# Performance work log

Measured on AMD Instinct MI355X. Metric: run time of the kernel, lower is better.

The kernel has to match this reference:

```python
import jax, jax.numpy as jnp
import numpy as np

N_NODES = 100000
N_GRAPHS = 256
HIDDEN = 64
IN_DIM = 512


def gcn_conv(x, edge_index, W, b, n_nodes):
    """PyG GCNConv: out = D^{-1/2} (A+I) D^{-1/2} (x W) + b."""
    h = x @ W  # [N, H] -- transform first (as PyG does), messages are small
    src = jnp.concatenate([edge_index[0], jnp.arange(n_nodes)])  # add self loops
    dst = jnp.concatenate([edge_index[1], jnp.arange(n_nodes)])
    ones = jnp.ones(src.shape[0], dtype=h.dtype)
    deg = jax.ops.segment_sum(ones, dst, num_segments=n_nodes)
    dinv = jnp.where(deg > 0, jax.lax.rsqrt(deg), 0.0)
    norm = dinv[src] * dinv[dst]  # [E+N]
    msg = h[src] * norm[:, None]  # gather + scale
    out = jax.ops.segment_sum(msg, dst, num_segments=n_nodes)  # scatter-add
    return out + b


def global_mean_pool(x, batch, num_graphs):
    s = jax.ops.segment_sum(x, batch, num_segments=num_graphs)
    cnt = jax.ops.segment_sum(jnp.ones(x.shape[0], dtype=x.dtype), batch,
                              num_segments=num_graphs)
    return s / jnp.maximum(cnt, 1.0)[:, None]


def setup_inputs() -> dict:
    key = jax.random.key(0)
    ks = jax.random.split(key, 9)
    x = jax.random.normal(ks[0], (N_NODES, IN_DIM), dtype=jnp.float32)
    edge_index = jax.random.randint(ks[1], (2, 1600000), 0, N_NODES, dtype=jnp.int64) \
        if jax.config.jax_enable_x64 else jax.random.randint(ks[1], (2, 1600000), 0, N_NODES).astype(jnp.int32)
    batch = jnp.sort(jax.random.randint(ks[2], (N_NODES,), 0, N_GRAPHS))
    sc1 = 1.0 / np.sqrt(IN_DIM)
    sc2 = 1.0 / np.sqrt(HIDDEN)
    W1 = jax.random.uniform(ks[3], (IN_DIM, HIDDEN), minval=-sc1, maxval=sc1, dtype=jnp.float32)
    b1 = jnp.zeros((HIDDEN,), dtype=jnp.float32)
    W2 = jax.random.uniform(ks[4], (HIDDEN, HIDDEN), minval=-sc2, maxval=sc2, dtype=jnp.float32)
    b2 = jnp.zeros((HIDDEN,), dtype=jnp.float32)
    Wfc = jax.random.uniform(ks[5], (HIDDEN, 1), minval=-sc2, maxval=sc2, dtype=jnp.float32)
    bfc = jnp.zeros((1,), dtype=jnp.float32)
    return {"x": x, "edge_index": edge_index, "batch": batch,
            "W1": W1, "b1": b1, "W2": W2, "b2": b2, "Wfc": Wfc, "bfc": bfc}


def reference(x, edge_index, batch, W1, b1, W2, b2, Wfc, bfc):
    n = x.shape[0]
    h = jax.nn.relu(gcn_conv(x, edge_index, W1, b1, n))
    h = jax.nn.relu(gcn_conv(h, edge_index, W2, b2, n))
    g = global_mean_pool(h, batch, N_GRAPHS)  # [G, H]
    out = g @ Wfc + bfc  # [G, 1]
    return out.squeeze(-1)
```

## Files before the change

### kernel.cpp

```cpp
#include <hip/hip_runtime.h>

#define HIDDEN 64
#define IN_DIM 512
#define CAP 4096
#define NB_MAX 1024

typedef short v8s __attribute__((ext_vector_type(8)));
typedef float v4f __attribute__((ext_vector_type(4)));

static __device__ __forceinline__ unsigned short f2bf(float f) {
    unsigned int u = __float_as_uint(f);
    u = (u + 0x7FFF + ((u >> 16) & 1)) >> 16;
    return (unsigned short)u;
}
static __device__ __forceinline__ float bf2f(unsigned short u) {
    return __uint_as_float(((unsigned int)u) << 16);
}
static __device__ __forceinline__ float bflo(unsigned u) { return __uint_as_float(u << 16); }
static __device__ __forceinline__ float bfhi(unsigned u) { return __uint_as_float(u & 0xffff0000u); }

__global__ void k_init(int* cursor, float* gsum, int* gcnt,
                       unsigned short* bufA, unsigned short* bufB, int n_nodes) {
    int i = blockIdx.x * 256 + threadIdx.x;
    if (i < NB_MAX) cursor[i] = 0;
    if (i < 256) { gsum[i] = 0.f; gcnt[i] = 0; }
    if (i < 64) {
        bufA[(size_t)n_nodes * 64 + i] = 0;
        bufB[(size_t)n_nodes * 64 + i] = 0;
    }
}

__launch_bounds__(256)
__global__ void k_bin(const int* __restrict__ src, const int* __restrict__ dst,
                      int* cursor, unsigned* __restrict__ bucket_data, int n_edges) {
    __shared__ unsigned words[4096];
    __shared__ unsigned short binsh[4096];
    __shared__ int hist[NB_MAX];
    __shared__ int base[NB_MAX];
    const int tid = threadIdx.x;
    const int e0 = blockIdx.x * 4096;
    for (int i = tid; i < NB_MAX; i += 256) hist[i] = 0;
    __syncthreads();
    for (int i = tid; i < 4096; i += 256) {
        int e = e0 + i;
        if (e < n_edges) {
            int d = dst[e], s = src[e];
            words[i] = ((unsigned)s << 7) | (unsigned)(d & 127);
            int b = d >> 7;
            binsh[i] = (unsigned short)b;
            atomicAdd(&hist[b], 1);
        } else binsh[i] = 0xFFFFu;
    }
    __syncthreads();
    for (int b = tid; b < NB_MAX; b += 256) {
        int c = hist[b];
        base[b] = c ? atomicAdd(&cursor[b], c) : 0;
        hist[b] = 0;
    }
    __syncthreads();
    for (int i = tid; i < 4096; i += 256) {
        unsigned short b = binsh[i];
        if (b != 0xFFFFu) {
            int slot = atomicAdd(&hist[b], 1);
            int p = base[b] + slot;
            if (p < CAP) bucket_data[(size_t)b * CAP + p] = words[i];
        }
    }
}

__launch_bounds__(256)
__global__ void k_bexc(const int* __restrict__ cursor, int* __restrict__ bucket_base,
                       int* __restrict__ row_start, int n_nodes, int nbuck) {
    __shared__ int wsum[4];
    const int t = threadIdx.x, lane = t & 63, w = t >> 6;
    int v[4], s = 0;
#pragma unroll
    for (int k = 0; k < 4; ++k) {
        int i = t * 4 + k;
        int c = (i < nbuck) ? cursor[i] : 0;
        if (c > CAP) c = CAP;
        v[k] = s; s += c;
    }
    int inc = s;
#pragma unroll
    for (int off = 1; off < 64; off <<= 1) {
        int u = __shfl_up(inc, off, 64);
        if (lane >= off) inc += u;
    }
    if (lane == 63) wsum[w] = inc;
    __syncthreads();
    int cross = 0;
    for (int i = 0; i < w; ++i) cross += wsum[i];
    int b0 = cross + inc - s;
#pragma unroll
    for (int k = 0; k < 4; ++k) {
        int i = t * 4 + k;
        if (i < NB_MAX) bucket_base[i] = b0 + v[k];
    }
    if (t == 255) row_start[n_nodes] = cross + inc;
}

__launch_bounds__(256)
__global__ void k_csr(const unsigned* __restrict__ bucket_data, const int* __restrict__ cursor,
                      const int* __restrict__ bucket_base,
                      int* __restrict__ row_start, int* __restrict__ csr,
                      float* __restrict__ dinv, int n_nodes) {
    __shared__ unsigned words[CAP];
    __shared__ int cnt[128];
    __shared__ int loff[128];
    __shared__ int cur[128];
    __shared__ int w0sum;
    const int tid = threadIdx.x, bin = blockIdx.x, n0 = bin << 7;
    int c = cursor[bin]; if (c > CAP) c = CAP;
    const unsigned* bd = bucket_data + (size_t)bin * CAP;
    for (int i = tid; i < c; i += 256) words[i] = bd[i];
    if (tid < 128) { cnt[tid] = 0; cur[tid] = 0; }
    __syncthreads();
    for (int i = tid; i < c; i += 256) atomicAdd(&cnt[words[i] & 127], 1);
    __syncthreads();
    int val = 0, inc = 0;
    if (tid < 128) {
        const int lane = tid & 63;
        val = cnt[tid];
        inc = val;
#pragma unroll
        for (int off = 1; off < 64; off <<= 1) {
            int u = __shfl_up(inc, off, 64);
            if (lane >= off) inc += u;
        }
        if (tid == 63) w0sum = inc;
    }
    __syncthreads();
    if (tid < 128) {
        int excl = inc - val + ((tid >= 64) ? w0sum : 0);
        loff[tid] = excl;
        int n = n0 + tid;
        if (n < n_nodes) {
            row_start[n] = bucket_base[bin] + excl;
            dinv[n] = rsqrtf((float)(val + 1));
        }
    }
    __syncthreads();
    const int gbase = bucket_base[bin];
    for (int i = tid; i < c; i += 256) {
        unsigned wd = words[i];
        int d = wd & 127;
        int slot = atomicAdd(&cur[d], 1);
        csr[gbase + loff[d] + slot] = (int)(wd & 0xFFFFFF80u);
    }
}

__global__ void k_prep(const float* __restrict__ W1, const float* __restrict__ W2,
                       unsigned short* __restrict__ Wt, unsigned short* __restrict__ Wt2) {
    int idx = blockIdx.x * 256 + threadIdx.x;
    if (idx < HIDDEN * IN_DIM) {
        int n = idx >> 9, k = idx & 511;
        Wt[(size_t)n * 512 + k] = f2bf(W1[(size_t)k * 64 + n]);
    } else {
        int j = idx - HIDDEN * IN_DIM;
        int n = j >> 6, k = j & 63;
        Wt2[(size_t)n * 64 + k] = f2bf(W2[(size_t)k * 64 + n]);
    }
}

__launch_bounds__(256)
__global__ void k_gemm1m(const float* __restrict__ x, const unsigned short* __restrict__ Wt,
                         const float* __restrict__ dinv, unsigned short* __restrict__ s1,
                         int n_nodes) {
    __shared__ __align__(16) unsigned short lX[64 * 136];
    __shared__ __align__(16) unsigned short lW[64 * 136];
    const int tid  = threadIdx.x;
    const int lane = tid & 63;
    const int w    = tid >> 6;
    const int quad = lane >> 4;
    const int m16  = lane & 15;
    const int row0 = blockIdx.x * 64;

    v4f acc[4];
#pragma unroll
    for (int b = 0; b < 4; ++b) acc[b] = (v4f){0.f, 0.f, 0.f, 0.f};

    for (int kc = 0; kc < IN_DIM; kc += 128) {
        __syncthreads();
#pragma unroll
        for (int i = 0; i < 8; ++i) {
            int fidx = tid + i * 256;
            int r  = fidx >> 5;
            int c4 = fidx & 31;
            int gr = row0 + r;
            float4 v = make_float4(0.f, 0.f, 0.f, 0.f);
            if (gr < n_nodes) v = ((const float4*)(x + (size_t)gr * IN_DIM + kc))[c4];
            ushort4 u = make_ushort4(f2bf(v.x), f2bf(v.y), f2bf(v.z), f2bf(v.w));
            *(ushort4*)(lX + r * 136 + c4 * 4) = u;
        }
#pragma unroll
        for (int i = 0; i < 4; ++i) {
            int idx = tid + i * 256;
            int n  = idx >> 4;
            int c8 = idx & 15;
            uint4 u = *(const uint4*)(Wt + (size_t)n * 512 + kc + c8 * 8);
            *(uint4*)(lW + n * 136 + c8 * 8) = u;
        }
        __syncthreads();
#pragma unroll
        for (int kk = 0; kk < 128; kk += 32) {
            v8s a = *(const v8s*)(lX + (w * 16 + m16) * 136 + kk + quad * 8);
#pragma unroll
            for (int b = 0; b < 4; ++b) {
                v8s bb = *(const v8s*)(lW + (b * 16 + m16) * 136 + kk + quad * 8);
                acc[b] = __builtin_amdgcn_mfma_f32_16x16x32_bf16(a, bb, acc[b], 0, 0, 0);
            }
        }
    }
    __syncthreads();
    float* lC = (float*)lX;
#pragma unroll
    for (int b = 0; b < 4; ++b)
#pragma unroll
        for (int r = 0; r < 4; ++r) {
            int rowt = w * 16 + quad * 4 + r;
            lC[rowt * 65 + b * 16 + m16] = acc[b][r];
        }
    __syncthreads();
#pragma unroll
    for (int i = 0; i < 2; ++i) {
        int base = i * 2048 + tid * 8;
        int r = base >> 6;
        int c = base & 63;
        int gr = row0 + r;
        if (gr < n_nodes) {
            float d = dinv[gr];
            const float* p = lC + r * 65 + c;
            unsigned p0 = (unsigned)f2bf(p[0] * d) | ((unsigned)f2bf(p[1] * d) << 16);
            unsigned p1 = (unsigned)f2bf(p[2] * d) | ((unsigned)f2bf(p[3] * d) << 16);
            unsigned p2 = (unsigned)f2bf(p[4] * d) | ((unsigned)f2bf(p[5] * d) << 16);
            unsigned p3 = (unsigned)f2bf(p[6] * d) | ((unsigned)f2bf(p[7] * d) << 16);
            *(uint4*)(s1 + (size_t)gr * 64 + c) = make_uint4(p0, p1, p2, p3);
        }
    }
}

__launch_bounds__(256)
__global__ void k_agg1g2(const unsigned short* __restrict__ sin, const int* __restrict__ row_start,
                         const int* __restrict__ csr, const float* __restrict__ dinv,
                         const unsigned short* __restrict__ Wt2, const float* __restrict__ b1,
                         unsigned short* __restrict__ sout, int n_nodes) {
    __shared__ __align__(16) unsigned short lW[64 * 72];
    __shared__ __align__(16) unsigned short lA[32 * 72];
    __shared__ __align__(16) float lC[32 * 65];
    const int tid  = threadIdx.x;
    const int lane = tid & 63;
    const int wave = tid >> 6;
    const int g = lane >> 3;
    const int l = lane & 7;
    const int row0 = blockIdx.x * 32;
    const int n = row0 + wave * 8 + g;
    const bool valid = (n < n_nodes);
    const char* sp = (const char*)sin;
    const int SENTB = n_nodes << 7;

#pragma unroll
    for (int i = 0; i < 2; ++i) {
        int idx = tid + i * 256;
        int nn = idx >> 3;
        int c8 = idx & 7;
        uint4 u = *(const uint4*)(Wt2 + (size_t)nn * 64 + c8 * 8);
        *(uint4*)(lW + nn * 72 + c8 * 8) = u;
    }

    int rs = 0, re = 0;
    if (valid) { rs = row_start[n]; re = row_start[n + 1]; }

    uint4 us = *(const uint4*)(sp + (size_t)(valid ? (n << 7) : SENTB) + l * 16);
    float acc0 = bflo(us.x), acc1 = bfhi(us.x);
    float acc2 = bflo(us.y), acc3 = bfhi(us.y);
    float acc4 = bflo(us.z), acc5 = bfhi(us.z);
    float acc6 = bflo(us.w), acc7 = bfhi(us.w);

    for (int base = rs; base < re; base += 16) {
        int p0 = base + l;
        int p1 = base + 8 + l;
        int a0 = (p0 < re) ? csr[p0] : SENTB;
        int a1 = (p1 < re) ? csr[p1] : SENTB;
#pragma unroll
        for (int j = 0; j < 8; ++j) {
            int ab = __shfl(a0, g * 8 + j, 64);
            uint4 u = *(const uint4*)(sp + (size_t)(unsigned)ab + l * 16);
            acc0 += bflo(u.x); acc1 += bfhi(u.x);
            acc2 += bflo(u.y); acc3 += bfhi(u.y);
            acc4 += bflo(u.z); acc5 += bfhi(u.z);
            acc6 += bflo(u.w); acc7 += bfhi(u.w);
        }
#pragma unroll
        for (int j = 0; j < 8; ++j) {
            int ab = __shfl(a1, g * 8 + j, 64);
            uint4 u = *(const uint4*)(sp + (size_t)(unsigned)ab + l * 16);
            acc0 += bflo(u.x); acc1 += bfhi(u.x);
            acc2 += bflo(u.y); acc3 += bfhi(u.y);
            acc4 += bflo(u.z); acc5 += bfhi(u.z);
            acc6 += bflo(u.w); acc7 += bfhi(u.w);
        }
    }
    {
        float d = valid ? dinv[n] : 0.f;
        const float4 bA = ((const float4*)b1)[2 * l];
        const float4 bB = ((const float4*)b1)[2 * l + 1];
        float t0 = d * acc0, t1 = d * acc1, t2 = d * acc2, t3 = d * acc3;
        float t4 = d * acc4, t5 = d * acc5, t6 = d * acc6, t7 = d * acc7;
        float v0 = fmaxf(t0 + bA.x, 0.f), v1 = fmaxf(t1 + bA.y, 0.f);
        float v2 = fmaxf(t2 + bA.z, 0.f), v3 = fmaxf(t3 + bA.w, 0.f);
        float v4 = fmaxf(t4 + bB.x, 0.f), v5 = fmaxf(t5 + bB.y, 0.f);
        float v6 = fmaxf(t6 + bB.z, 0.f), v7 = fmaxf(t7 + bB.w, 0.f);
        unsigned q0 = (unsigned)f2bf(v0) | ((unsigned)f2bf(v1) << 16);
        unsigned q1 = (unsigned)f2bf(v2) | ((unsigned)f2bf(v3) << 16);
        unsigned q2 = (unsigned)f2bf(v4) | ((unsigned)f2bf(v5) << 16);
        unsigned q3 = (unsigned)f2bf(v6) | ((unsigned)f2bf(v7) << 16);
        int r = wave * 8 + g;
        *(uint4*)(lA + r * 72 + l * 8) = make_uint4(q0, q1, q2, q3);
    }
    __syncthreads();
    {
        const int m16  = lane & 15;
        const int quad = lane >> 4;
        const int mt  = wave >> 1;
        const int nt0 = (wave & 1) * 2;
        v4f c0 = (v4f){0.f, 0.f, 0.f, 0.f};
        v4f c1 = (v4f){0.f, 0.f, 0.f, 0.f};
#pragma unroll
        for (int kk = 0; kk < 64; kk += 32) {
            v8s a  = *(const v8s*)(lA + (mt * 16 + m16) * 72 + kk + quad * 8);
            v8s b0 = *(const v8s*)(lW + (nt0 * 16 + m16) * 72 + kk + quad * 8);
            v8s b1v = *(const v8s*)(lW + ((nt0 + 1) * 16 + m16) * 72 + kk + quad * 8);
            c0 = __builtin_amdgcn_mfma_f32_16x16x32_bf16(a, b0, c0, 0, 0, 0);
            c1 = __builtin_amdgcn_mfma_f32_16x16x32_bf16(a, b1v, c1, 0, 0, 0);
        }
#pragma unroll
        for (int r = 0; r < 4; ++r) {
            int rowt = mt * 16 + quad * 4 + r;
            lC[rowt * 65 + nt0 * 16 + m16]       = c0[r];
            lC[rowt * 65 + (nt0 + 1) * 16 + m16] = c1[r];
        }
    }
    __syncthreads();
    {
        int base = tid * 8;
        int r = base >> 6;
        int c = base & 63;
        int gr = row0 + r;
        if (gr < n_nodes) {
            float d = dinv[gr];
            const float* p = lC + r * 65 + c;
            unsigned p0 = (unsigned)f2bf(p[0] * d) | ((unsigned)f2bf(p[1] * d) << 16);
            unsigned p1 = (unsigned)f2bf(p[2] * d) | ((unsigned)f2bf(p[3] * d) << 16);
            unsigned p2 = (unsigned)f2bf(p[4] * d) | ((unsigned)f2bf(p[5] * d) << 16);
            unsigned p3 = (unsigned)f2bf(p[6] * d) | ((unsigned)f2bf(p[7] * d) << 16);
            *(uint4*)(sout + (size_t)gr * 64 + c) = make_uint4(p0, p1, p2, p3);
        }
    }
}

__launch_bounds__(256)
__global__ void k_layer2pool(const unsigned short* __restrict__ sin, const int* __restrict__ row_start,
                             const int* __restrict__ csr, const float* __restrict__ b2,
                             const float* __restrict__ dinv, const float* __restrict__ Wfc,
                             const int* __restrict__ batch,
                             float* gsum, int* gcnt, int n_nodes) {
    __shared__ float lsum[256];
    __shared__ int   lcnt[256];
    const int tid = threadIdx.x;
    lsum[tid] = 0.f; lcnt[tid] = 0;
    __syncthreads();
    const int lane = tid & 63;
    const int wave = tid >> 6;
    const int g = lane >> 3;
    const int l = lane & 7;
    const int n = (blockIdx.x * 4 + wave) * 8 + g;
    const bool valid = (n < n_nodes);
    const char* sp = (const char*)sin;
    const int SENTB = n_nodes << 7;

    int rs = 0, re = 0;
    if (valid) { rs = row_start[n]; re = row_start[n + 1]; }

    uint4 us = *(const uint4*)(sp + (size_t)(valid ? (n << 7) : SENTB) + l * 16);
    float acc0 = bflo(us.x), acc1 = bfhi(us.x);
    float acc2 = bflo(us.y), acc3 = bfhi(us.y);
    float acc4 = bflo(us.z), acc5 = bfhi(us.z);
    float acc6 = bflo(us.w), acc7 = bfhi(us.w);

    for (int base = rs; base < re; base += 16) {
        int p0 = base + l;
        int p1 = base + 8 + l;
        int a0 = (p0 < re) ? csr[p0] : SENTB;
        int a1 = (p1 < re) ? csr[p1] : SENTB;
#pragma unroll
        for (int j = 0; j < 8; ++j) {
            int ab = __shfl(a0, g * 8 + j, 64);
            uint4 u = *(const uint4*)(sp + (size_t)(unsigned)ab + l * 16);
            acc0 += bflo(u.x); acc1 += bfhi(u.x);
            acc2 += bflo(u.y); acc3 += bfhi(u.y);
            acc4 += bflo(u.z); acc5 += bfhi(u.z);
            acc6 += bflo(u.w); acc7 += bfhi(u.w);
        }
#pragma unroll
        for (int j = 0; j < 8; ++j) {
            int ab = __shfl(a1, g * 8 + j, 64);
            uint4 u = *(const uint4*)(sp + (size_t)(unsigned)ab + l * 16);
            acc0 += bflo(u.x); acc1 += bfhi(u.x);
            acc2 += bflo(u.y); acc3 += bfhi(u.y);
            acc4 += bflo(u.z); acc5 += bfhi(u.z);
            acc6 += bflo(u.w); acc7 += bfhi(u.w);
        }
    }
    float d = dinv[valid ? n : 0];
    const float4 bA  = ((const float4*)b2)[2 * l];
    const float4 bB  = ((const float4*)b2)[2 * l + 1];
    const float4 wA  = ((const float4*)Wfc)[2 * l];
    const float4 wB  = ((const float4*)Wfc)[2 * l + 1];
    float t = fmaxf(fmaf(d, acc0, bA.x), 0.f) * wA.x
            + fmaxf(fmaf(d, acc1, bA.y), 0.f) * wA.y
            + fmaxf(fmaf(d, acc2, bA.z), 0.f) * wA.z
            + fmaxf(fmaf(d, acc3, bA.w), 0.f) * wA.w
            + fmaxf(fmaf(d, acc4, bB.x), 0.f) * wB.x
            + fmaxf(fmaf(d, acc5, bB.y), 0.f) * wB.y
            + fmaxf(fmaf(d, acc6, bB.z), 0.f) * wB.z
            + fmaxf(fmaf(d, acc7, bB.w), 0.f) * wB.w;
#pragma unroll
    for (int off = 4; off; off >>= 1) t += __shfl_down(t, off, 8);
    if (l == 0 && valid) {
        int gr = batch[n];
        atomicAdd(&lsum[gr], t);
        atomicAdd(&lcnt[gr], 1);
    }
    __syncthreads();
    if (lcnt[tid]) {
        atomicAdd(&gsum[tid], lsum[tid]);
        atomicAdd(&gcnt[tid], lcnt[tid]);
    }
}

__global__ void k_out(const float* __restrict__ gsum, const int* __restrict__ gcnt,
                      const float* __restrict__ bfc, float* out) {
    int g = threadIdx.x;
    if (g < 256) {
        float c = (float)(gcnt[g] > 1 ? gcnt[g] : 1);
        out[g] = gsum[g] / c + bfc[0];
    }
}

extern "C" void kernel_launch(void* const* d_in, const int* in_sizes, int n_in,
                              void* d_out, int out_size, void* d_ws, size_t ws_size,
                              hipStream_t stream) {
    const float* x   = (const float*)d_in[0];
    const int*   ei  = (const int*)d_in[1];
    const int*   bat = (const int*)d_in[2];
    const float* W1  = (const float*)d_in[3];
    const float* b1  = (const float*)d_in[4];
    const float* W2  = (const float*)d_in[5];
    const float* b2  = (const float*)d_in[6];
    const float* Wfc = (const float*)d_in[7];
    const float* bfc = (const float*)d_in[8];
    float* out = (float*)d_out;

    const int n_nodes = in_sizes[2];
    const int n_edges = in_sizes[1] / 2;
    const int* src = ei;
    const int* dst = ei + n_edges;
    const int NBUCK = (n_nodes + 127) >> 7;

    char* w = (char*)d_ws;
    size_t off = 0;
    auto alloc = [&](size_t bytes) -> void* {
        void* p = w + off;
        off += (bytes + 255) & ~(size_t)255;
        return p;
    };
    float* dinv = (float*)alloc((size_t)n_nodes * sizeof(float));
    unsigned short* bufA = (unsigned short*)alloc(((size_t)n_nodes + 1) * HIDDEN * 2);
    unsigned short* bufB = (unsigned short*)alloc(((size_t)n_nodes + 1) * HIDDEN * 2);
    unsigned short* Wt   = (unsigned short*)alloc((size_t)HIDDEN * IN_DIM * 2);
    unsigned short* Wt2  = (unsigned short*)alloc((size_t)HIDDEN * HIDDEN * 2);
    float* gsum = (float*)alloc(256 * sizeof(float));
    int*   gcnt = (int*)  alloc(256 * sizeof(int));
    int*   cursor      = (int*)alloc((size_t)NB_MAX * sizeof(int));
    int*   bucket_base = (int*)alloc((size_t)NB_MAX * sizeof(int));
    unsigned* bucket_data = (unsigned*)alloc((size_t)NB_MAX * CAP * sizeof(unsigned));
    int* row_start = (int*)alloc(((size_t)n_nodes + 1) * sizeof(int));
    int* csr       = (int*)alloc(((size_t)n_edges + 64) * sizeof(int));
    (void)ws_size; (void)n_in; (void)out_size;

    hipLaunchKernelGGL(k_init, dim3(NB_MAX / 256), dim3(256), 0, stream,
                       cursor, gsum, gcnt, bufA, bufB, n_nodes);
    hipLaunchKernelGGL(k_bin, dim3((n_edges + 4095) / 4096), dim3(256), 0, stream,
                       src, dst, cursor, bucket_data, n_edges);
    hipLaunchKernelGGL(k_bexc, dim3(1), dim3(256), 0, stream,
                       cursor, bucket_base, row_start, n_nodes, NBUCK);
    hipLaunchKernelGGL(k_csr, dim3(NBUCK), dim3(256), 0, stream,
                       bucket_data, cursor, bucket_base, row_start, csr, dinv, n_nodes);
    hipLaunchKernelGGL(k_prep, dim3((HIDDEN * IN_DIM + HIDDEN * HIDDEN) / 256), dim3(256), 0, stream,
                       W1, W2, Wt, Wt2);
    hipLaunchKernelGGL(k_gemm1m, dim3((n_nodes + 63) / 64), dim3(256), 0, stream,
                       x, Wt, dinv, bufA, n_nodes);
    hipLaunchKernelGGL(k_agg1g2, dim3((n_nodes + 31) / 32), dim3(256), 0, stream,
                       bufA, row_start, csr, dinv, Wt2, b1, bufB, n_nodes);
    hipLaunchKernelGGL(k_layer2pool, dim3((n_nodes + 31) / 32), dim3(256), 0, stream,
                       bufB, row_start, csr, b2, dinv, Wfc, bat, gsum, gcnt, n_nodes);
    hipLaunchKernelGGL(k_out, dim3(1), dim3(256), 0, stream, gsum, gcnt, bfc, out);
}
```

Measured before the change: 415.3 us.

## Sort nodes by degree bucket to balance aggregation wave workloads

Builds a degree histogram during CSR construction, scans it, and produces a permutation that groups nodes with similar in-degree. Both aggregation kernels then process nodes in this permuted order, so the 8 nodes sharing a wave have similar edge counts and less lane divergence. This adds two small kernels and an extra indirection per node, and it scatters the output writes and the batch/dinv reads, which costs memory locality.

```diff
diff --git a/kernel.cpp b/kernel.cpp
--- a/kernel.cpp
+++ b/kernel.cpp
@@ -4,6 +4,7 @@
 #define IN_DIM 512
 #define CAP 4096
 #define NB_MAX 1024
+#define DBINS 512
 
 typedef short v8s __attribute__((ext_vector_type(8)));
 typedef float v4f __attribute__((ext_vector_type(4)));
@@ -20,10 +21,11 @@
 static __device__ __forceinline__ float bfhi(unsigned u) { return __uint_as_float(u & 0xffff0000u); }
 
 __global__ void k_init(int* cursor, float* gsum, int* gcnt,
-                       unsigned short* bufA, unsigned short* bufB, int n_nodes) {
+                       unsigned short* bufA, unsigned short* bufB, int* ghist, int n_nodes) {
     int i = blockIdx.x * 256 + threadIdx.x;
     if (i < NB_MAX) cursor[i] = 0;
     if (i < 256) { gsum[i] = 0.f; gcnt[i] = 0; }
+    if (i < DBINS) ghist[i] = 0;
     if (i < 64) {
         bufA[(size_t)n_nodes * 64 + i] = 0;
         bufB[(size_t)n_nodes * 64 + i] = 0;
@@ -104,17 +106,19 @@
 __global__ void k_csr(const unsigned* __restrict__ bucket_data, const int* __restrict__ cursor,
                       const int* __restrict__ bucket_base,
                       int* __restrict__ row_start, int* __restrict__ csr,
-                      float* __restrict__ dinv, int n_nodes) {
+                      float* __restrict__ dinv, int* __restrict__ ghist, int n_nodes) {
     __shared__ unsigned words[CAP];
     __shared__ int cnt[128];
     __shared__ int loff[128];
     __shared__ int cur[128];
+    __shared__ int dhist[DBINS];
     __shared__ int w0sum;
     const int tid = threadIdx.x, bin = blockIdx.x, n0 = bin << 7;
     int c = cursor[bin]; if (c > CAP) c = CAP;
     const unsigned* bd = bucket_data + (size_t)bin * CAP;
     for (int i = tid; i < c; i += 256) words[i] = bd[i];
     if (tid < 128) { cnt[tid] = 0; cur[tid] = 0; }
+    for (int i = tid; i < DBINS; i += 256) dhist[i] = 0;
     __syncthreads();
     for (int i = tid; i < c; i += 256) atomicAdd(&cnt[words[i] & 127], 1);
     __syncthreads();
@@ -138,15 +142,75 @@
         if (n < n_nodes) {
             row_start[n] = bucket_base[bin] + excl;
             dinv[n] = rsqrtf((float)(val + 1));
-        }
-    }
-    __syncthreads();
+            int cb = (val + 15) >> 4;
+            atomicAdd(&dhist[cb], 1);
+        }
+    }
+    __syncthreads();
+    for (int b = tid; b < DBINS; b += 256)
+        if (dhist[b]) atomicAdd(&ghist[b], dhist[b]);
     const int gbase = bucket_base[bin];
     for (int i = tid; i < c; i += 256) {
         unsigned wd = words[i];
         int d = wd & 127;
         int slot = atomicAdd(&cur[d], 1);
         csr[gbase + loff[d] + slot] = (int)(wd & 0xFFFFFF80u);
+    }
+}
+
+__launch_bounds__(256)
+__global__ void k_cscan(const int* __restrict__ ghist, int* __restrict__ dcur) {
+    __shared__ int wsum[4];
+    const int t = threadIdx.x, lane = t & 63, w = t >> 6;
+    int v0 = ghist[2 * t], v1 = ghist[2 * t + 1];
+    int s = v0 + v1;
+    int inc = s;
+#pragma unroll
+    for (int off = 1; off < 64; off <<= 1) {
+        int u = __shfl_up(inc, off, 64);
+        if (lane >= off) inc += u;
+    }
+    if (lane == 63) wsum[w] = inc;
+    __syncthreads();
+    int cross = 0;
+    for (int i = 0; i < w; ++i) cross += wsum[i];
+    int b0 = cross + inc - s;
+    dcur[2 * t] = b0;
+    dcur[2 * t + 1] = b0 + v0;
+}
+
+__launch_bounds__(256)
+__global__ void k_cplace(const int* __restrict__ row_start, int* dcur,
+                         int* __restrict__ perm, int n_nodes) {
+    __shared__ int lh[DBINS];
+    __shared__ int lbase[DBINS];
+    __shared__ int lcur[DBINS];
+    const int tid = threadIdx.x;
+    const int n0 = blockIdx.x * 4096;
+    for (int i = tid; i < DBINS; i += 256) lh[i] = 0;
+    __syncthreads();
+    for (int i = tid; i < 4096; i += 256) {
+        int n = n0 + i;
+        if (n < n_nodes) {
+            int deg = row_start[n + 1] - row_start[n];
+            atomicAdd(&lh[(deg + 15) >> 4], 1);
+        }
+    }
+    __syncthreads();
+    for (int b = tid; b < DBINS; b += 256) {
+        int cnt = lh[b];
+        lbase[b] = cnt ? atomicAdd(&dcur[b], cnt) : 0;
+        lcur[b] = 0;
+    }
+    __syncthreads();
+    for (int i = tid; i < 4096; i += 256) {
+        int n = n0 + i;
+        if (n < n_nodes) {
+            int deg = row_start[n + 1] - row_start[n];
+            int cb = (deg + 15) >> 4;
+            int slot = atomicAdd(&lcur[cb], 1);
+            perm[lbase[cb] + slot] = n;
+        }
     }
 }
 
@@ -244,6 +308,7 @@
 __global__ void k_agg1g2(const unsigned short* __restrict__ sin, const int* __restrict__ row_start,
                          const int* __restrict__ csr, const float* __restrict__ dinv,
                          const unsigned short* __restrict__ Wt2, const float* __restrict__ b1,
+                         const int* __restrict__ perm,
                          unsigned short* __restrict__ sout, int n_nodes) {
     __shared__ __align__(16) unsigned short lW[64 * 72];
     __shared__ __align__(16) unsigned short lA[32 * 72];
@@ -254,8 +319,9 @@
     const int g = lane >> 3;
     const int l = lane & 7;
     const int row0 = blockIdx.x * 32;
-    const int n = row0 + wave * 8 + g;
-    const bool valid = (n < n_nodes);
+    const int gid = row0 + wave * 8 + g;
+    const bool valid = (gid < n_nodes);
+    const int n = valid ? perm[gid] : 0;
     const char* sp = (const char*)sin;
     const int SENTB = n_nodes << 7;
 
@@ -346,8 +412,9 @@
         int base = tid * 8;
         int r = base >> 6;
         int c = base & 63;
-        int gr = row0 + r;
-        if (gr < n_nodes) {
+        int gid2 = row0 + r;
+        if (gid2 < n_nodes) {
+            int gr = perm[gid2];
             float d = dinv[gr];
             const float* p = lC + r * 65 + c;
             unsigned p0 = (unsigned)f2bf(p[0] * d) | ((unsigned)f2bf(p[1] * d) << 16);
@@ -363,7 +430,7 @@
 __global__ void k_layer2pool(const unsigned short* __restrict__ sin, const int* __restrict__ row_start,
                              const int* __restrict__ csr, const float* __restrict__ b2,
                              const float* __restrict__ dinv, const float* __restrict__ Wfc,
-                             const int* __restrict__ batch,
+                             const int* __restrict__ batch, const int* __restrict__ perm,
                              float* gsum, int* gcnt, int n_nodes) {
     __shared__ float lsum[256];
     __shared__ int   lcnt[256];
@@ -374,8 +441,9 @@
     const int wave = tid >> 6;
     const int g = lane >> 3;
     const int l = lane & 7;
-    const int n = (blockIdx.x * 4 + wave) * 8 + g;
-    const bool valid = (n < n_nodes);
+    const int gid = (blockIdx.x * 4 + wave) * 8 + g;
+    const bool valid = (gid < n_nodes);
+    const int n = valid ? perm[gid] : 0;
     const char* sp = (const char*)sin;
     const int SENTB = n_nodes << 7;
 
@@ -412,7 +480,7 @@
             acc6 += bflo(u.w); acc7 += bfhi(u.w);
         }
     }
-    float d = dinv[valid ? n : 0];
+    float d = dinv[n];
     const float4 bA  = ((const float4*)b2)[2 * l];
     const float4 bB  = ((const float4*)b2)[2 * l + 1];
     const float4 wA  = ((const float4*)Wfc)[2 * l];
@@ -484,26 +552,32 @@
     int*   gcnt = (int*)  alloc(256 * sizeof(int));
     int*   cursor      = (int*)alloc((size_t)NB_MAX * sizeof(int));
     int*   bucket_base = (int*)alloc((size_t)NB_MAX * sizeof(int));
+    int*   ghist       = (int*)alloc((size_t)DBINS * sizeof(int));
+    int*   dcur        = (int*)alloc((size_t)DBINS * sizeof(int));
+    int*   perm        = (int*)alloc((size_t)n_nodes * sizeof(int));
     unsigned* bucket_data = (unsigned*)alloc((size_t)NB_MAX * CAP * sizeof(unsigned));
     int* row_start = (int*)alloc(((size_t)n_nodes + 1) * sizeof(int));
     int* csr       = (int*)alloc(((size_t)n_edges + 64) * sizeof(int));
     (void)ws_size; (void)n_in; (void)out_size;
 
     hipLaunchKernelGGL(k_init, dim3(NB_MAX / 256), dim3(256), 0, stream,
-                       cursor, gsum, gcnt, bufA, bufB, n_nodes);
+                       cursor, gsum, gcnt, bufA, bufB, ghist, n_nodes);
     hipLaunchKernelGGL(k_bin, dim3((n_edges + 4095) / 4096), dim3(256), 0, stream,
                        src, dst, cursor, bucket_data, n_edges);
     hipLaunchKernelGGL(k_bexc, dim3(1), dim3(256), 0, stream,
                        cursor, bucket_base, row_start, n_nodes, NBUCK);
     hipLaunchKernelGGL(k_csr, dim3(NBUCK), dim3(256), 0, stream,
-                       bucket_data, cursor, bucket_base, row_start, csr, dinv, n_nodes);
+                       bucket_data, cursor, bucket_base, row_start, csr, dinv, ghist, n_nodes);
+    hipLaunchKernelGGL(k_cscan, dim3(1), dim3(256), 0, stream, ghist, dcur);
+    hipLaunchKernelGGL(k_cplace, dim3((n_nodes + 4095) / 4096), dim3(256), 0, stream,
+                       row_start, dcur, perm, n_nodes);
     hipLaunchKernelGGL(k_prep, dim3((HIDDEN * IN_DIM + HIDDEN * HIDDEN) / 256), dim3(256), 0, stream,
                        W1, W2, Wt, Wt2);
     hipLaunchKernelGGL(k_gemm1m, dim3((n_nodes + 63) / 64), dim3(256), 0, stream,
                        x, Wt, dinv, bufA, n_nodes);
     hipLaunchKernelGGL(k_agg1g2, dim3((n_nodes + 31) / 32), dim3(256), 0, stream,
-                       bufA, row_start, csr, dinv, Wt2, b1, bufB, n_nodes);
+                       bufA, row_start, csr, dinv, Wt2, b1, perm, bufB, n_nodes);
     hipLaunchKernelGGL(k_layer2pool, dim3((n_nodes + 31) / 32), dim3(256), 0, stream,
-                       bufB, row_start, csr, b2, dinv, Wfc, bat, gsum, gcnt, n_nodes);
+                       bufB, row_start, csr, b2, dinv, Wfc, bat, perm, gsum, gcnt, n_nodes);
     hipLaunchKernelGGL(k_out, dim3(1), dim3(256), 0, stream, gsum, gcnt, bfc, out);
 }
```

Measured after the change: 434.5 us. 1.05x slower.

## Partition CSR neighbor lists into four source-range slices for gather locality

Applied to the files above, without the earlier changes.

The CSR build now sub-sorts each node's neighbors into four slices by source node index and records four segment starts per node in a new rs4 array. Both aggregation kernels walk these segments in order, so waves running at the same time tend to gather from the same quarter of the feature table, which may improve L2 hit rates. The gather loop also changes from 16 edges per iteration to 8, with the next index block prefetched. The cost is four tail-padded segments per node instead of one, which means more masked sentinel loads for low-degree nodes, plus extra atomics and shared memory in the CSR build.

```diff
diff --git a/kernel.cpp b/kernel.cpp
--- a/kernel.cpp
+++ b/kernel.cpp
@@ -70,7 +70,8 @@
 
 __launch_bounds__(256)
 __global__ void k_bexc(const int* __restrict__ cursor, int* __restrict__ bucket_base,
-                       int* __restrict__ row_start, int n_nodes, int nbuck) {
+                       int* __restrict__ row_start, int* __restrict__ rs4,
+                       int n_nodes, int nbuck) {
     __shared__ int wsum[4];
     const int t = threadIdx.x, lane = t & 63, w = t >> 6;
     int v[4], s = 0;
@@ -97,31 +98,42 @@
         int i = t * 4 + k;
         if (i < NB_MAX) bucket_base[i] = b0 + v[k];
     }
-    if (t == 255) row_start[n_nodes] = cross + inc;
+    if (t == 255) {
+        row_start[n_nodes] = cross + inc;
+        rs4[4 * n_nodes]   = cross + inc;
+    }
 }
 
 __launch_bounds__(256)
 __global__ void k_csr(const unsigned* __restrict__ bucket_data, const int* __restrict__ cursor,
                       const int* __restrict__ bucket_base,
-                      int* __restrict__ row_start, int* __restrict__ csr,
-                      float* __restrict__ dinv, int n_nodes) {
+                      int* __restrict__ row_start, int* __restrict__ rs4, int* __restrict__ csr,
+                      float* __restrict__ dinv, int n_nodes, float inv_slice) {
     __shared__ unsigned words[CAP];
-    __shared__ int cnt[128];
-    __shared__ int loff[128];
-    __shared__ int cur[128];
+    __shared__ int cnt4[512];
+    __shared__ int loff4[512];
+    __shared__ int cur4[512];
     __shared__ int w0sum;
     const int tid = threadIdx.x, bin = blockIdx.x, n0 = bin << 7;
     int c = cursor[bin]; if (c > CAP) c = CAP;
     const unsigned* bd = bucket_data + (size_t)bin * CAP;
     for (int i = tid; i < c; i += 256) words[i] = bd[i];
-    if (tid < 128) { cnt[tid] = 0; cur[tid] = 0; }
-    __syncthreads();
-    for (int i = tid; i < c; i += 256) atomicAdd(&cnt[words[i] & 127], 1);
-    __syncthreads();
-    int val = 0, inc = 0;
+    for (int i = tid; i < 512; i += 256) { cnt4[i] = 0; cur4[i] = 0; }
+    __syncthreads();
+    for (int i = tid; i < c; i += 256) {
+        unsigned wd = words[i];
+        int d = wd & 127;
+        int q = (int)((float)(wd >> 7) * inv_slice);
+        q = q > 3 ? 3 : q;
+        atomicAdd(&cnt4[d * 4 + q], 1);
+    }
+    __syncthreads();
+    int v0 = 0, v1 = 0, v2 = 0, v3 = 0, val = 0, inc = 0;
     if (tid < 128) {
         const int lane = tid & 63;
-        val = cnt[tid];
+        v0 = cnt4[tid * 4]; v1 = cnt4[tid * 4 + 1];
+        v2 = cnt4[tid * 4 + 2]; v3 = cnt4[tid * 4 + 3];
+        val = v0 + v1 + v2 + v3;
         inc = val;
 #pragma unroll
         for (int off = 1; off < 64; off <<= 1) {
@@ -133,10 +145,17 @@
     __syncthreads();
     if (tid < 128) {
         int excl = inc - val + ((tid >= 64) ? w0sum : 0);
-        loff[tid] = excl;
+        int B = bucket_base[bin];
+        loff4[tid * 4]     = excl;
+        loff4[tid * 4 + 1] = excl + v0;
+        loff4[tid * 4 + 2] = excl + v0 + v1;
+        loff4[tid * 4 + 3] = excl + v0 + v1 + v2;
         int n = n0 + tid;
         if (n < n_nodes) {
-            row_start[n] = bucket_base[bin] + excl;
+            row_start[n] = B + excl;
+            int4 r4 = make_int4(B + excl, B + excl + v0,
+                                B + excl + v0 + v1, B + excl + v0 + v1 + v2);
+            *(int4*)(rs4 + 4 * n) = r4;
             dinv[n] = rsqrtf((float)(val + 1));
         }
     }
@@ -145,8 +164,10 @@
     for (int i = tid; i < c; i += 256) {
         unsigned wd = words[i];
         int d = wd & 127;
-        int slot = atomicAdd(&cur[d], 1);
-        csr[gbase + loff[d] + slot] = (int)(wd & 0xFFFFFF80u);
+        int q = (int)((float)(wd >> 7) * inv_slice);
+        q = q > 3 ? 3 : q;
+        int slot = atomicAdd(&cur4[d * 4 + q], 1);
+        csr[gbase + loff4[d * 4 + q] + slot] = (int)(wd & 0xFFFFFF80u);
     }
 }
 
@@ -241,7 +262,7 @@
 }
 
 __launch_bounds__(256)
-__global__ void k_agg1g2(const unsigned short* __restrict__ sin, const int* __restrict__ row_start,
+__global__ void k_agg1g2(const unsigned short* __restrict__ sin, const int* __restrict__ rs4,
                          const int* __restrict__ csr, const float* __restrict__ dinv,
                          const unsigned short* __restrict__ Wt2, const float* __restrict__ b1,
                          unsigned short* __restrict__ sout, int n_nodes) {
@@ -268,8 +289,12 @@
         *(uint4*)(lW + nn * 72 + c8 * 8) = u;
     }
 
-    int rs = 0, re = 0;
-    if (valid) { rs = row_start[n]; re = row_start[n + 1]; }
+    int4 r4 = make_int4(0, 0, 0, 0);
+    int rend = 0;
+    if (valid) {
+        r4 = *(const int4*)(rs4 + 4 * n);
+        rend = rs4[4 * n + 4];
+    }
 
     uint4 us = *(const uint4*)(sp + (size_t)(valid ? (n << 7) : SENTB) + l * 16);
     float acc0 = bflo(us.x), acc1 = bfhi(us.x);
@@ -277,30 +302,28 @@
     float acc4 = bflo(us.z), acc5 = bfhi(us.z);
     float acc6 = bflo(us.w), acc7 = bfhi(us.w);
 
-    for (int base = rs; base < re; base += 16) {
-        int p0 = base + l;
-        int p1 = base + 8 + l;
-        int a0 = (p0 < re) ? csr[p0] : SENTB;
-        int a1 = (p1 < re) ? csr[p1] : SENTB;
-#pragma unroll
-        for (int j = 0; j < 8; ++j) {
-            int ab = __shfl(a0, g * 8 + j, 64);
-            uint4 u = *(const uint4*)(sp + (size_t)(unsigned)ab + l * 16);
-            acc0 += bflo(u.x); acc1 += bfhi(u.x);
-            acc2 += bflo(u.y); acc3 += bfhi(u.y);
-            acc4 += bflo(u.z); acc5 += bfhi(u.z);
-            acc6 += bflo(u.w); acc7 += bfhi(u.w);
-        }
-#pragma unroll
-        for (int j = 0; j < 8; ++j) {
-            int ab = __shfl(a1, g * 8 + j, 64);
-            uint4 u = *(const uint4*)(sp + (size_t)(unsigned)ab + l * 16);
-            acc0 += bflo(u.x); acc1 += bfhi(u.x);
-            acc2 += bflo(u.y); acc3 += bfhi(u.y);
-            acc4 += bflo(u.z); acc5 += bfhi(u.z);
-            acc6 += bflo(u.w); acc7 += bfhi(u.w);
-        }
-    }
+    auto gather_seg = [&](int rs, int re) {
+        int a0 = (rs + l < re) ? csr[rs + l] : SENTB;
+        for (int base = rs; base < re; base += 8) {
+            int nb = base + 8;
+            int na0 = (nb + l < re) ? csr[nb + l] : SENTB;
+#pragma unroll
+            for (int j = 0; j < 8; ++j) {
+                int ab = __shfl(a0, g * 8 + j, 64);
+                uint4 u = *(const uint4*)(sp + (size_t)(unsigned)ab + l * 16);
+                acc0 += bflo(u.x); acc1 += bfhi(u.x);
+                acc2 += bflo(u.y); acc3 += bfhi(u.y);
+                acc4 += bflo(u.z); acc5 += bfhi(u.z);
+                acc6 += bflo(u.w); acc7 += bfhi(u.w);
+            }
+            a0 = na0;
+        }
+    };
+    gather_seg(r4.x, r4.y);
+    gather_seg(r4.y, r4.z);
+    gather_seg(r4.z, r4.w);
+    gather_seg(r4.w, rend);
+
     {
         float d = valid ? dinv[n] : 0.f;
         const float4 bA = ((const float4*)b1)[2 * l];
@@ -360,7 +383,7 @@
 }
 
 __launch_bounds__(256)
-__global__ void k_layer2pool(const unsigned short* __restrict__ sin, const int* __restrict__ row_start,
+__global__ void k_layer2pool(const unsigned short* __restrict__ sin, const int* __restrict__ rs4,
                              const int* __restrict__ csr, const float* __restrict__ b2,
                              const float* __restrict__ dinv, const float* __restrict__ Wfc,
                              const int* __restrict__ batch,
@@ -379,8 +402,12 @@
     const char* sp = (const char*)sin;
     const int SENTB = n_nodes << 7;
 
-    int rs = 0, re = 0;
-    if (valid) { rs = row_start[n]; re = row_start[n + 1]; }
+    int4 r4 = make_int4(0, 0, 0, 0);
+    int rend = 0;
+    if (valid) {
+        r4 = *(const int4*)(rs4 + 4 * n);
+        rend = rs4[4 * n + 4];
+    }
 
     uint4 us = *(const uint4*)(sp + (size_t)(valid ? (n << 7) : SENTB) + l * 16);
     float acc0 = bflo(us.x), acc1 = bfhi(us.x);
@@ -388,30 +415,28 @@
     float acc4 = bflo(us.z), acc5 = bfhi(us.z);
     float acc6 = bflo(us.w), acc7 = bfhi(us.w);
 
-    for (int base = rs; base < re; base += 16) {
-        int p0 = base + l;
-        int p1 = base + 8 + l;
-        int a0 = (p0 < re) ? csr[p0] : SENTB;
-        int a1 = (p1 < re) ? csr[p1] : SENTB;
-#pragma unroll
-        for (int j = 0; j < 8; ++j) {
-            int ab = __shfl(a0, g * 8 + j, 64);
-            uint4 u = *(const uint4*)(sp + (size_t)(unsigned)ab + l * 16);
-            acc0 += bflo(u.x); acc1 += bfhi(u.x);
-            acc2 += bflo(u.y); acc3 += bfhi(u.y);
-            acc4 += bflo(u.z); acc5 += bfhi(u.z);
-            acc6 += bflo(u.w); acc7 += bfhi(u.w);
-        }
-#pragma unroll
-        for (int j = 0; j < 8; ++j) {
-            int ab = __shfl(a1, g * 8 + j, 64);
-            uint4 u = *(const uint4*)(sp + (size_t)(unsigned)ab + l * 16);
-            acc0 += bflo(u.x); acc1 += bfhi(u.x);
-            acc2 += bflo(u.y); acc3 += bfhi(u.y);
-            acc4 += bflo(u.z); acc5 += bfhi(u.z);
-            acc6 += bflo(u.w); acc7 += bfhi(u.w);
-        }
-    }
+    auto gather_seg = [&](int rs, int re) {
+        int a0 = (rs + l < re) ? csr[rs + l] : SENTB;
+        for (int base = rs; base < re; base += 8) {
+            int nb = base + 8;
+            int na0 = (nb + l < re) ? csr[nb + l] : SENTB;
+#pragma unroll
+            for (int j = 0; j < 8; ++j) {
+                int ab = __shfl(a0, g * 8 + j, 64);
+                uint4 u = *(const uint4*)(sp + (size_t)(unsigned)ab + l * 16);
+                acc0 += bflo(u.x); acc1 += bfhi(u.x);
+                acc2 += bflo(u.y); acc3 += bfhi(u.y);
+                acc4 += bflo(u.z); acc5 += bfhi(u.z);
+                acc6 += bflo(u.w); acc7 += bfhi(u.w);
+            }
+            a0 = na0;
+        }
+    };
+    gather_seg(r4.x, r4.y);
+    gather_seg(r4.y, r4.z);
+    gather_seg(r4.z, r4.w);
+    gather_seg(r4.w, rend);
+
     float d = dinv[valid ? n : 0];
     const float4 bA  = ((const float4*)b2)[2 * l];
     const float4 bB  = ((const float4*)b2)[2 * l + 1];
@@ -467,6 +492,8 @@
     const int* src = ei;
     const int* dst = ei + n_edges;
     const int NBUCK = (n_nodes + 127) >> 7;
+    const int slice_rows = (n_nodes + 3) >> 2;
+    const float inv_slice = 1.0f / (float)slice_rows;
 
     char* w = (char*)d_ws;
     size_t off = 0;
@@ -484,6 +511,7 @@
     int*   gcnt = (int*)  alloc(256 * sizeof(int));
     int*   cursor      = (int*)alloc((size_t)NB_MAX * sizeof(int));
     int*   bucket_base = (int*)alloc((size_t)NB_MAX * sizeof(int));
+    int*   rs4         = (int*)alloc(((size_t)n_nodes * 4 + 4) * sizeof(int));
     unsigned* bucket_data = (unsigned*)alloc((size_t)NB_MAX * CAP * sizeof(unsigned));
     int* row_start = (int*)alloc(((size_t)n_nodes + 1) * sizeof(int));
     int* csr       = (int*)alloc(((size_t)n_edges + 64) * sizeof(int));
@@ -494,16 +522,17 @@
     hipLaunchKernelGGL(k_bin, dim3((n_edges + 4095) / 4096), dim3(256), 0, stream,
                        src, dst, cursor, bucket_data, n_edges);
     hipLaunchKernelGGL(k_bexc, dim3(1), dim3(256), 0, stream,
-                       cursor, bucket_base, row_start, n_nodes, NBUCK);
+                       cursor, bucket_base, row_start, rs4, n_nodes, NBUCK);
     hipLaunchKernelGGL(k_csr, dim3(NBUCK), dim3(256), 0, stream,
-                       bucket_data, cursor, bucket_base, row_start, csr, dinv, n_nodes);
+                       bucket_data, cursor, bucket_base, row_start, rs4, csr, dinv,
+                       n_nodes, inv_slice);
     hipLaunchKernelGGL(k_prep, dim3((HIDDEN * IN_DIM + HIDDEN * HIDDEN) / 256), dim3(256), 0, stream,
                        W1, W2, Wt, Wt2);
     hipLaunchKernelGGL(k_gemm1m, dim3((n_nodes + 63) / 64), dim3(256), 0, stream,
                        x, Wt, dinv, bufA, n_nodes);
     hipLaunchKernelGGL(k_agg1g2, dim3((n_nodes + 31) / 32), dim3(256), 0, stream,
-                       bufA, row_start, csr, dinv, Wt2, b1, bufB, n_nodes);
+                       bufA, rs4, csr, dinv, Wt2, b1, bufB, n_nodes);
     hipLaunchKernelGGL(k_layer2pool, dim3((n_nodes + 31) / 32), dim3(256), 0, stream,
-                       bufB, row_start, csr, b2, dinv, Wfc, bat, gsum, gcnt, n_nodes);
+                       bufB, rs4, csr, b2, dinv, Wfc, bat, gsum, gcnt, n_nodes);
     hipLaunchKernelGGL(k_out, dim3(1), dim3(256), 0, stream, gsum, gcnt, bfc, out);
 }
```

Result: no change. 413.8 us (-0.4%).
